# Kernel tuning notes

Hardware: AMD Instinct MI355X
Metric: run time of the kernel (lower is better)

## Reference

```python
import jax, jax.numpy as jnp
import numpy as np

N = 64       # number of nodes (features)
K = 512      # sequence length
WIN = 5
KS = 5       # conv kernel size
EMBED = 64   # embed_dim


def setup_inputs() -> dict:
    key = jax.random.key(0)
    ks = jax.random.split(key, 8)
    x = jax.random.normal(ks[0], (N, K), dtype=jnp.float32)
    # fully connected graph without self loops (remove_self_loops is then a no-op)
    src, dst = np.nonzero(~np.eye(N, dtype=bool))
    edge_index = jnp.asarray(np.stack([src, dst]), dtype=jnp.int32)  # [2, E]
    conv_w = jax.random.normal(ks[1], (1, 1, KS), dtype=jnp.float32) * 0.3
    conv_b = jnp.zeros((1,), jnp.float32)
    s = 1.0 / np.sqrt(WIN)
    lin_l_w = jax.random.uniform(ks[2], (EMBED, WIN), jnp.float32, -s, s)
    lin_l_b = jax.random.uniform(ks[3], (EMBED,), jnp.float32, -s, s)
    lin_r_w = jax.random.uniform(ks[4], (EMBED, WIN), jnp.float32, -s, s)
    lin_r_b = jax.random.uniform(ks[5], (EMBED,), jnp.float32, -s, s)
    glorot = np.sqrt(6.0 / (1 + EMBED))
    att = jax.random.uniform(ks[6], (1, EMBED), jnp.float32, -glorot, glorot)
    return dict(x=x, edge_index=edge_index, conv_w=conv_w, conv_b=conv_b,
                lin_l_w=lin_l_w, lin_l_b=lin_l_b, lin_r_w=lin_r_w,
                lin_r_b=lin_r_b, att=att)


def reference(x, edge_index, conv_w, conv_b, lin_l_w, lin_l_b, lin_r_w, lin_r_b, att):
    n_temp = K - WIN + 1
    # Conv1d(1,1,KS, padding='same') + sigmoid
    h = jax.lax.conv_general_dilated(x[:, None, :], conv_w, window_strides=(1,),
                                     padding='SAME',
                                     dimension_numbers=('NCH', 'OIH', 'NCH'))
    h = jax.nn.sigmoid(h[:, 0, :] + conv_b)                      # [N, K]
    widx = jnp.arange(n_temp)[:, None] + jnp.arange(WIN)[None, :]
    xw = h[:, widx].reshape(-1, WIN)
    # temporal edge index: node idx -> idx*n_temp + t
    t = jnp.arange(n_temp)[None, :]
    l = (edge_index[0][:, None] * n_temp + t).reshape(-1)        # [E*n_temp]
    r = (edge_index[1][:, None] * n_temp + t).reshape(-1)
    x_l = xw @ lin_l_w.T + lin_l_b                               # [N*n_temp, EMBED]
    x_r = xw @ lin_r_w.T + lin_r_b
    e = jax.nn.leaky_relu(x_l[l] + x_r[r], negative_slope=0.2)   # [E*n_temp, EMBED]
    alpha = (e * att).sum(-1)                                    # [E*n_temp]
    # segment softmax grouped by source temporal node l
    S = N * n_temp
    m = jax.ops.segment_max(alpha, l, num_segments=S)
    a = jnp.exp(alpha - m[l])
    denom = jax.ops.segment_sum(a, l, num_segments=S)
    alpha = a / (denom[l] + 1e-16)
    return alpha.reshape(-1, n_temp)                             # [E, n_temp]
```

## Files before the change

### kernel.cpp

```cpp
#include <hip/hip_runtime.h>

#define NNODE 64
#define KLEN  512
#define WIN   5
#define NT    508
#define EMB   64
#define NDST  63
#define ETOT  4032
#define XRP   68

__global__ __launch_bounds__(256) void attn_fused(
    const float* __restrict__ x,
    const float* __restrict__ conv_w,
    const float* __restrict__ conv_b,
    const float* __restrict__ lin_l_w,
    const float* __restrict__ lin_l_b,
    const float* __restrict__ lin_r_w,
    const float* __restrict__ lin_r_b,
    const float* __restrict__ att,
    float* __restrict__ out)
{
    const int bx = blockIdx.x;
    const int t  = (bx & 7) * 64 + (bx >> 3);
    if (t >= NT) return;
    const int sg   = blockIdx.y;
    const int tid  = threadIdx.x;
    const int lane = tid & 63;
    const int wave = tid >> 6;

    __shared__ float h_s[NNODE][WIN];
    __shared__ float xr_s[NNODE][XRP];
    __shared__ float xl_s[16][EMB];
    __shared__ float att_s[EMB];

    if (tid < EMB) att_s[tid] = att[tid];

    for (int idx = tid; idx < NNODE * WIN; idx += 256) {
        const int n = idx / WIN;
        const int w = idx % WIN;
        const int base = t + w - 2;
        float acc = conv_b[0];
        #pragma unroll
        for (int j = 0; j < WIN; ++j) {
            const int k = base + j;
            const float xv = (k >= 0 && k < KLEN) ? x[n * KLEN + k] : 0.f;
            acc = fmaf(conv_w[j], xv, acc);
        }
        h_s[n][w] = 1.f / (1.f + __expf(-acc));
    }
    __syncthreads();

    {
        float rw[WIN];
        #pragma unroll
        for (int w = 0; w < WIN; ++w) rw[w] = lin_r_w[lane * WIN + w];
        const float rb = lin_r_b[lane];
        #pragma unroll
        for (int k = 0; k < 16; ++k) {
            const int r = wave + k * 4;
            float acc = rb;
            #pragma unroll
            for (int w = 0; w < WIN; ++w)
                acc = fmaf(rw[w], h_s[r][w], acc);
            xr_s[r][lane] = acc;
        }
    }
    {
        float lw[WIN];
        #pragma unroll
        for (int w = 0; w < WIN; ++w) lw[w] = lin_l_w[lane * WIN + w];
        const float lb = lin_l_b[lane];
        #pragma unroll
        for (int k = 0; k < 4; ++k) {
            const int sl = wave + k * 4;
            const int s  = sg * 16 + sl;
            float acc = lb;
            #pragma unroll
            for (int w = 0; w < WIN; ++w)
                acc = fmaf(lw[w], h_s[s][w], acc);
            xl_s[sl][lane] = acc;
        }
    }
    __syncthreads();

    float accm[4] = {0.f, 0.f, 0.f, 0.f};
    const float* xrrow = &xr_s[lane][0];
    #pragma unroll 4
    for (int d0 = 0; d0 < EMB; d0 += 4) {
        const float4 xr4 = *(const float4*)(xrrow + d0);
        const float4 at4 = *(const float4*)(&att_s[d0]);
        #pragma unroll
        for (int p = 0; p < 4; ++p) {
            const float4 xl4 = *(const float4*)(&xl_s[wave * 4 + p][d0]);
            float z, zm;
            z = xl4.x + xr4.x; zm = fminf(z, 0.f);
            accm[p] = fmaf(at4.x, fmaf(-0.8f, zm, z), accm[p]);
            z = xl4.y + xr4.y; zm = fminf(z, 0.f);
            accm[p] = fmaf(at4.y, fmaf(-0.8f, zm, z), accm[p]);
            z = xl4.z + xr4.z; zm = fminf(z, 0.f);
            accm[p] = fmaf(at4.z, fmaf(-0.8f, zm, z), accm[p]);
            z = xl4.w + xr4.w; zm = fminf(z, 0.f);
            accm[p] = fmaf(at4.w, fmaf(-0.8f, zm, z), accm[p]);
        }
    }

    #pragma unroll
    for (int p = 0; p < 4; ++p) {
        const int s = sg * 16 + wave * 4 + p;
        float alpha = accm[p];
        if (lane == s) alpha = -INFINITY;
        float m = alpha;
        #pragma unroll
        for (int off = 32; off; off >>= 1) m = fmaxf(m, __shfl_xor(m, off));
        float ex = __expf(alpha - m);
        if (lane == s) ex = 0.f;
        float sum = ex;
        #pragma unroll
        for (int off = 32; off; off >>= 1) sum += __shfl_xor(sum, off);
        const float res = ex / (sum + 1e-16f);
        if (lane != s) {
            const int j = lane - (lane > s ? 1 : 0);
            const int e = s * NDST + j;
            out[(size_t)e * NT + t] = res;
        }
    }
}

extern "C" void kernel_launch(void* const* d_in, const int* in_sizes, int n_in,
                              void* d_out, int out_size, void* d_ws, size_t ws_size,
                              hipStream_t stream)
{
    const float* x       = (const float*)d_in[0];
    const float* conv_w  = (const float*)d_in[2];
    const float* conv_b  = (const float*)d_in[3];
    const float* lin_l_w = (const float*)d_in[4];
    const float* lin_l_b = (const float*)d_in[5];
    const float* lin_r_w = (const float*)d_in[6];
    const float* lin_r_b = (const float*)d_in[7];
    const float* att     = (const float*)d_in[8];
    float* out = (float*)d_out;

    attn_fused<<<dim3(512, 4), 256, 0, stream>>>(x, conv_w, conv_b,
        lin_l_w, lin_l_b, lin_r_w, lin_r_b, att, out);
}
```

Before: 30.78 us.

## Split leaky-relu attention into linear part plus min term, broadcast xl via readlane

```diff
diff --git a/kernel.cpp b/kernel.cpp
--- a/kernel.cpp
+++ b/kernel.cpp
@@ -6,8 +6,11 @@
 #define NT    508
 #define EMB   64
 #define NDST  63
-#define ETOT  4032
 #define XRP   68
+
+__device__ __forceinline__ float readlane_f(float v, int l) {
+    return __int_as_float(__builtin_amdgcn_readlane(__float_as_int(v), l));
+}
 
 __global__ __launch_bounds__(256) void attn_fused(
     const float* __restrict__ x,
@@ -28,12 +31,8 @@
     const int lane = tid & 63;
     const int wave = tid >> 6;
 
-    __shared__ float h_s[NNODE][WIN];
+    __shared__ float h_s[NNODE][8];
     __shared__ float xr_s[NNODE][XRP];
-    __shared__ float xl_s[16][EMB];
-    __shared__ float att_s[EMB];
-
-    if (tid < EMB) att_s[tid] = att[tid];
 
     for (int idx = tid; idx < NNODE * WIN; idx += 256) {
         const int n = idx / WIN;
@@ -50,6 +49,8 @@
     }
     __syncthreads();
 
+    const float attv = att[lane];
+
     {
         float rw[WIN];
         #pragma unroll
@@ -65,49 +66,61 @@
             xr_s[r][lane] = acc;
         }
     }
+
+    float xlv[4], A[4];
     {
         float lw[WIN];
         #pragma unroll
         for (int w = 0; w < WIN; ++w) lw[w] = lin_l_w[lane * WIN + w];
         const float lb = lin_l_b[lane];
         #pragma unroll
-        for (int k = 0; k < 4; ++k) {
-            const int sl = wave + k * 4;
-            const int s  = sg * 16 + sl;
+        for (int p = 0; p < 4; ++p) {
+            const int s = sg * 16 + wave * 4 + p;
             float acc = lb;
             #pragma unroll
             for (int w = 0; w < WIN; ++w)
                 acc = fmaf(lw[w], h_s[s][w], acc);
-            xl_s[sl][lane] = acc;
+            xlv[p] = acc;
+            float v = attv * acc;
+            #pragma unroll
+            for (int off = 32; off; off >>= 1) v += __shfl_xor(v, off);
+            A[p] = v;
         }
     }
     __syncthreads();
 
     float accm[4] = {0.f, 0.f, 0.f, 0.f};
+    float accB = 0.f;
     const float* xrrow = &xr_s[lane][0];
-    #pragma unroll 4
+    #pragma unroll
     for (int d0 = 0; d0 < EMB; d0 += 4) {
         const float4 xr4 = *(const float4*)(xrrow + d0);
-        const float4 at4 = *(const float4*)(&att_s[d0]);
+        const float a0 = att[d0 + 0];
+        const float a1 = att[d0 + 1];
+        const float a2 = att[d0 + 2];
+        const float a3 = att[d0 + 3];
+        accB = fmaf(a0, xr4.x, accB);
+        accB = fmaf(a1, xr4.y, accB);
+        accB = fmaf(a2, xr4.z, accB);
+        accB = fmaf(a3, xr4.w, accB);
         #pragma unroll
         for (int p = 0; p < 4; ++p) {
-            const float4 xl4 = *(const float4*)(&xl_s[wave * 4 + p][d0]);
-            float z, zm;
-            z = xl4.x + xr4.x; zm = fminf(z, 0.f);
-            accm[p] = fmaf(at4.x, fmaf(-0.8f, zm, z), accm[p]);
-            z = xl4.y + xr4.y; zm = fminf(z, 0.f);
-            accm[p] = fmaf(at4.y, fmaf(-0.8f, zm, z), accm[p]);
-            z = xl4.z + xr4.z; zm = fminf(z, 0.f);
-            accm[p] = fmaf(at4.z, fmaf(-0.8f, zm, z), accm[p]);
-            z = xl4.w + xr4.w; zm = fminf(z, 0.f);
-            accm[p] = fmaf(at4.w, fmaf(-0.8f, zm, z), accm[p]);
+            float z;
+            z = readlane_f(xlv[p], d0 + 0) + xr4.x;
+            accm[p] = fmaf(a0, fminf(z, 0.f), accm[p]);
+            z = readlane_f(xlv[p], d0 + 1) + xr4.y;
+            accm[p] = fmaf(a1, fminf(z, 0.f), accm[p]);
+            z = readlane_f(xlv[p], d0 + 2) + xr4.z;
+            accm[p] = fmaf(a2, fminf(z, 0.f), accm[p]);
+            z = readlane_f(xlv[p], d0 + 3) + xr4.w;
+            accm[p] = fmaf(a3, fminf(z, 0.f), accm[p]);
         }
     }
 
     #pragma unroll
     for (int p = 0; p < 4; ++p) {
         const int s = sg * 16 + wave * 4 + p;
-        float alpha = accm[p];
+        float alpha = fmaf(-0.8f, accm[p], A[p] + accB);
         if (lane == s) alpha = -INFINITY;
         float m = alpha;
         #pragma unroll
```

Result: slower. 34.73 us (+12.8%).
